# Kernel optimization log

Measured on AMD Instinct MI355X. Metric: run time of the kernel, lower is better.

The kernel has to match this reference:

```python
import jax, jax.numpy as jnp
import numpy as np


def setup_inputs() -> dict:
    key = jax.random.key(0)
    k0, k1, k2, k3, k4 = jax.random.split(key, 5)
    n, c, s, h, w = 4, 128, 31, 32, 22
    x = jax.random.normal(k0, (n, c, s, h, w), dtype=jnp.float32)
    # 1x1 conv to a single channel == per-pixel dot over channels + scalar bias
    scale = 1.0 / np.sqrt(c).astype(np.float32)
    w1 = jax.random.normal(k1, (c,), dtype=jnp.float32) * scale
    b1 = jax.random.normal(k2, (), dtype=jnp.float32) * 0.01
    w2 = jax.random.normal(k3, (c,), dtype=jnp.float32) * scale
    b2 = jax.random.normal(k4, (), dtype=jnp.float32) * 0.01
    return {"x": x, "w1": w1, "b1": b1, "w2": w2, "b2": b2, "top_k": 16}


def reference(x, w1, b1, w2, b2, top_k):
    n, c, s, h, w = x.shape
    hw = h * w
    ns = n * (s - 1)
    # adjacent-frame pairs; 1x1 conv (C->1) as channel contraction
    X0 = jnp.einsum('ncshw,c->nshw', x[:, :, : s - 1], w1) + b1  # (n, s-1, h, w)
    X1 = jnp.einsum('ncshw,c->nshw', x[:, :, 1:], w2) + b2       # (n, s-1, h, w)
    X0 = X0.reshape(ns, hw)
    X1 = X1.reshape(ns, hw)
    # outer-product scores per frame pair, softmax over last dim
    attention = jax.nn.softmax(X0[:, :, None] * X1[:, None, :], axis=2)  # (ns, hw, hw)
    # top-k values along last dim -> (ns, hw, k); torch .view(ns, k, h, w)
    # is a raw row-major reinterpretation, so a plain reshape is faithful.
    vals, _ = jax.lax.top_k(attention, top_k)
    vals = vals.reshape(n, s - 1, top_k, h, w)
    # trans_out: (n, s-1, k, h, w) -> (n, k, s-1, h, w)
    return jnp.transpose(vals, (0, 2, 1, 3, 4))
```

## Files before the change

kernel.cpp:

```cpp
#include <hip/hip_runtime.h>
#include <math.h>

#define NB   4
#define C    128
#define S    31
#define HW   704
#define T    30
#define NS   120
#define K    16

__global__ __launch_bounds__(256) void conv_select_kernel(
    const float* __restrict__ x,
    const float* __restrict__ w1, const float* __restrict__ b1p,
    const float* __restrict__ w2, const float* __restrict__ b2p,
    float* __restrict__ A, float* __restrict__ B,
    float* __restrict__ ptop, float* __restrict__ pbot) {
  const int tid   = threadIdx.x;
  const int lane  = tid & 63;
  const int cg    = tid >> 6;
  const int fr    = blockIdx.x / 3;
  const int chunk = blockIdx.x % 3;
  const int sf    = fr % S;
  const int n     = fr / S;
  const int f4    = chunk * 64 + lane;
  const bool act  = f4 < 176;
  const int f4c   = act ? f4 : 175;

  const float4* xp =
      (const float4*)(x + (((size_t)(n * C + cg * 32) * S + sf) * HW)) + f4c;
  float4 a1 = make_float4(0.f, 0.f, 0.f, 0.f);
  float4 a2 = make_float4(0.f, 0.f, 0.f, 0.f);
#pragma unroll
  for (int c = 0; c < 32; ++c) {
    float4 xv = xp[(size_t)c * (S * HW / 4)];
    const float wa = w1[cg * 32 + c];
    const float wb = w2[cg * 32 + c];
    a1.x = fmaf(xv.x, wa, a1.x); a1.y = fmaf(xv.y, wa, a1.y);
    a1.z = fmaf(xv.z, wa, a1.z); a1.w = fmaf(xv.w, wa, a1.w);
    a2.x = fmaf(xv.x, wb, a2.x); a2.y = fmaf(xv.y, wb, a2.y);
    a2.z = fmaf(xv.z, wb, a2.z); a2.w = fmaf(xv.w, wb, a2.w);
  }
  __shared__ float4 s1[4][64];
  __shared__ float4 s2[4][64];
  s1[cg][lane] = a1;
  s2[cg][lane] = a2;
  __syncthreads();
  if (tid < 64) {
    float4 r1 = s1[0][tid], r2 = s2[0][tid];
#pragma unroll
    for (int u = 1; u < 4; ++u) {
      float4 t1 = s1[u][tid], t2 = s2[u][tid];
      r1.x += t1.x; r1.y += t1.y; r1.z += t1.z; r1.w += t1.w;
      r2.x += t2.x; r2.y += t2.y; r2.z += t2.z; r2.w += t2.w;
    }
    const float bb1 = b1p[0], bb2 = b2p[0];
    r1.x += bb1; r1.y += bb1; r1.z += bb1; r1.w += bb1;
    r2.x += bb2; r2.y += bb2; r2.z += bb2; r2.w += bb2;
    const bool act2 = (chunk * 64 + tid) < 176;
    if (act2) {
      if (sf < T)
        ((float4*)(A + (size_t)(n * T + sf) * HW))[chunk * 64 + tid] = r1;
      if (sf >= 1)
        ((float4*)(B + (size_t)(n * T + sf - 1) * HW))[chunk * 64 + tid] = r2;
    }
    s2[0][tid] = r2;
  }
  __syncthreads();

  if (tid < 64 && sf >= 1) {
    const int i = n * T + sf - 1;
    const int nv = (chunk == 2) ? 3 : 4;
    const float* bs = (const float*)&s2[0][0];
    float vt[4], vb[4];
#pragma unroll
    for (int j = 0; j < 3; ++j) {
      const float v = bs[j * 64 + tid];
      vt[j] = v; vb[j] = v;
    }
    if (nv == 4) { const float v = bs[192 + tid]; vt[3] = v; vb[3] = v; }
    else         { vt[3] = -INFINITY;         vb[3] = INFINITY; }
    float* pt = ptop + (i * 3 + chunk) * K;
    float* pb = pbot + (i * 3 + chunk) * K;
#pragma unroll 1
    for (int rr = 0; rr < K; ++rr) {
      float lmT = fmaxf(fmaxf(vt[0], vt[1]), fmaxf(vt[2], vt[3]));
      float lmB = fminf(fminf(vb[0], vb[1]), fminf(vb[2], vb[3]));
      float gT = lmT, gB = lmB;
#pragma unroll
      for (int off = 1; off < 64; off <<= 1) {
        gT = fmaxf(gT, __shfl_xor(gT, off, 64));
        gB = fminf(gB, __shfl_xor(gB, off, 64));
      }
      const unsigned long long mT = __ballot(lmT == gT);
      const unsigned long long mB = __ballot(lmB == gB);
      if (tid == (int)(__ffsll(mT) - 1)) {
        bool done = false;
#pragma unroll
        for (int j = 0; j < 4; ++j) {
          const bool hit = (!done) && (vt[j] == gT);
          vt[j] = hit ? -INFINITY : vt[j];
          done  = done || hit;
        }
      }
      if (tid == (int)(__ffsll(mB) - 1)) {
        bool done = false;
#pragma unroll
        for (int j = 0; j < 4; ++j) {
          const bool hit = (!done) && (vb[j] == gB);
          vb[j] = hit ? INFINITY : vb[j];
          done  = done || hit;
        }
      }
      if (tid == 0) { pt[rr] = gT; pb[rr] = gB; }
    }
  }
}

__global__ __launch_bounds__(256) void softmax_merge_kernel(
    const float* __restrict__ A, const float* __restrict__ B,
    const float* __restrict__ ptop, const float* __restrict__ pbot,
    float* __restrict__ out) {
  __shared__ float4 bs4[176];
  __shared__ float  partial[4][64];
  __shared__ float  seltop[K], selbot[K];
  const int tid  = threadIdx.x;
  const int lane = tid & 63;
  const int w    = tid >> 6;
  const int i    = blockIdx.x / 11;
  const int slab = blockIdx.x % 11;
  const int n    = i / T;
  const int tp   = i % T;

  if (tid < 176) bs4[tid] = ((const float4*)(B + i * HW))[tid];
  const int   r = slab * 64 + lane;
  const float a = A[i * HW + r];

  if (w == 0) {
    const float* pt = ptop + i * 3 * K;
    float e = -INFINITY;
    if (lane < 16)       e = pt[lane];
    else if (lane < 32)  e = pt[47 - lane];
#pragma unroll
    for (int off = 16; off >= 1; off >>= 1) {
      const float xx = __shfl_xor(e, off, 64);
      e = (lane & off) ? fminf(e, xx) : fmaxf(e, xx);
    }
    if (lane >= 32)      e = -INFINITY;
    else if (lane >= 16) e = pt[63 - lane];
#pragma unroll
    for (int off = 16; off >= 1; off >>= 1) {
      const float xx = __shfl_xor(e, off, 64);
      e = (lane & off) ? fminf(e, xx) : fmaxf(e, xx);
    }
    if (lane < 16) seltop[lane] = e;
  } else if (w == 1) {
    const float* pb = pbot + i * 3 * K;
    float e = INFINITY;
    if (lane < 16)       e = pb[lane];
    else if (lane < 32)  e = pb[47 - lane];
#pragma unroll
    for (int off = 16; off >= 1; off >>= 1) {
      const float xx = __shfl_xor(e, off, 64);
      e = (lane & off) ? fmaxf(e, xx) : fminf(e, xx);
    }
    if (lane >= 32)      e = INFINITY;
    else if (lane >= 16) e = pb[63 - lane];
#pragma unroll
    for (int off = 16; off >= 1; off >>= 1) {
      const float xx = __shfl_xor(e, off, 64);
      e = (lane & off) ? fmaxf(e, xx) : fminf(e, xx);
    }
    if (lane < 16) selbot[lane] = e;
  }
  __syncthreads();

  const float st0 = seltop[0];
  const float sb0 = selbot[0];
  const float L2E = 1.4426950408889634f;
  const float a2  = a * L2E;
  const float nm  = -((a >= 0.f) ? a * st0 : a * sb0) * L2E;

  float p0 = 0.f, p1 = 0.f, p2 = 0.f, p3 = 0.f;
#pragma unroll 11
  for (int j = 0; j < 44; ++j) {
    const float4 bq = bs4[w * 44 + j];
    p0 += __builtin_amdgcn_exp2f(fmaf(a2, bq.x, nm));
    p1 += __builtin_amdgcn_exp2f(fmaf(a2, bq.y, nm));
    p2 += __builtin_amdgcn_exp2f(fmaf(a2, bq.z, nm));
    p3 += __builtin_amdgcn_exp2f(fmaf(a2, bq.w, nm));
  }
  partial[w][lane] = (p0 + p1) + (p2 + p3);
  __syncthreads();

  if (w == 0) {
    const float part =
        (partial[0][lane] + partial[1][lane]) +
        (partial[2][lane] + partial[3][lane]);
    const float rp = 1.f / part;
    float ov[16];
#pragma unroll
    for (int t = 0; t < K; ++t) {
      const float sel = (a >= 0.f) ? seltop[t] : selbot[t];
      ov[t] = __builtin_amdgcn_exp2f(fmaf(a2, sel, nm)) * rp;
    }
    float* op = out + (((size_t)(n * K + r / 44)) * T + tp) * HW + (r % 44) * K;
#pragma unroll
    for (int t4 = 0; t4 < 4; ++t4)
      ((float4*)op)[t4] = ((const float4*)ov)[t4];
  }
}

extern "C" void kernel_launch(void* const* d_in, const int* in_sizes, int n_in,
                              void* d_out, int out_size, void* d_ws, size_t ws_size,
                              hipStream_t stream) {
  (void)in_sizes; (void)n_in; (void)out_size; (void)ws_size;
  const float* x  = (const float*)d_in[0];
  const float* w1 = (const float*)d_in[1];
  const float* b1 = (const float*)d_in[2];
  const float* w2 = (const float*)d_in[3];
  const float* b2 = (const float*)d_in[4];
  float* out = (float*)d_out;

  float* A    = (float*)d_ws;
  float* B    = A + NS * HW;
  float* ptop = B + NS * HW;
  float* pbot = ptop + NS * 3 * K;

  conv_select_kernel<<<372, 256, 0, stream>>>(x, w1, b1, w2, b2,
                                              A, B, ptop, pbot);
  softmax_merge_kernel<<<NS * 11, 256, 0, stream>>>(A, B, ptop, pbot, out);
}
```

Before: 107.5 us.

## Fuse conv/select and softmax kernels into one cooperative launch with grid sync

Merges the two kernels into a single cooperative kernel that runs the conv/partial-top-k phase on the first 372 blocks, then uses a grid-wide barrier before every block runs the softmax/merge phase. Shared memory for the two phases is overlaid in a union. This aims to remove the second kernel launch and the gap between launches. The cost is a grid.sync over 1320 blocks, which requires all blocks to be co-resident, plus the latency of the barrier itself. If the cooperative launch fails, the code falls back to the original two launches.

```diff
diff --git a/kernel.cpp b/kernel.cpp
--- a/kernel.cpp
+++ b/kernel.cpp
@@ -1,5 +1,8 @@
 #include <hip/hip_runtime.h>
+#include <hip/hip_cooperative_groups.h>
 #include <math.h>
+
+namespace cg = cooperative_groups;
 
 #define NB   4
 #define C    128
@@ -8,6 +11,212 @@
 #define T    30
 #define NS   120
 #define K    16
+#define CONVB 372
+#define GRID  (NS * 11)
+
+__global__ __launch_bounds__(256) void fused_kernel(
+    const float* __restrict__ x,
+    const float* __restrict__ w1, const float* __restrict__ b1p,
+    const float* __restrict__ w2, const float* __restrict__ b2p,
+    float* __restrict__ A, float* __restrict__ B,
+    float* __restrict__ ptop, float* __restrict__ pbot,
+    float* __restrict__ out) {
+  __shared__ union {
+    struct { float4 s1[4][64]; float4 s2[4][64]; } p1;
+    struct {
+      float4 bs4[176];
+      float  partial[4][64];
+      float  seltop[K], selbot[K];
+    } p2;
+  } sm;
+  cg::grid_group grid = cg::this_grid();
+  const int tid  = threadIdx.x;
+  const int lane = tid & 63;
+
+  if (blockIdx.x < CONVB) {
+    const int cg_   = tid >> 6;
+    const int fr    = blockIdx.x / 3;
+    const int chunk = blockIdx.x % 3;
+    const int sf    = fr % S;
+    const int n     = fr / S;
+    const int f4    = chunk * 64 + lane;
+    const int f4c   = (f4 < 176) ? f4 : 175;
+
+    const float4* xp =
+        (const float4*)(x + (((size_t)(n * C + cg_ * 32) * S + sf) * HW)) + f4c;
+    float4 a1 = make_float4(0.f, 0.f, 0.f, 0.f);
+    float4 a2 = make_float4(0.f, 0.f, 0.f, 0.f);
+#pragma unroll
+    for (int c = 0; c < 32; ++c) {
+      float4 xv = xp[(size_t)c * (S * HW / 4)];
+      const float wa = w1[cg_ * 32 + c];
+      const float wb = w2[cg_ * 32 + c];
+      a1.x = fmaf(xv.x, wa, a1.x); a1.y = fmaf(xv.y, wa, a1.y);
+      a1.z = fmaf(xv.z, wa, a1.z); a1.w = fmaf(xv.w, wa, a1.w);
+      a2.x = fmaf(xv.x, wb, a2.x); a2.y = fmaf(xv.y, wb, a2.y);
+      a2.z = fmaf(xv.z, wb, a2.z); a2.w = fmaf(xv.w, wb, a2.w);
+    }
+    sm.p1.s1[cg_][lane] = a1;
+    sm.p1.s2[cg_][lane] = a2;
+    __syncthreads();
+    if (tid < 64) {
+      float4 r1 = sm.p1.s1[0][tid], r2 = sm.p1.s2[0][tid];
+#pragma unroll
+      for (int u = 1; u < 4; ++u) {
+        float4 t1 = sm.p1.s1[u][tid], t2 = sm.p1.s2[u][tid];
+        r1.x += t1.x; r1.y += t1.y; r1.z += t1.z; r1.w += t1.w;
+        r2.x += t2.x; r2.y += t2.y; r2.z += t2.z; r2.w += t2.w;
+      }
+      const float bb1 = b1p[0], bb2 = b2p[0];
+      r1.x += bb1; r1.y += bb1; r1.z += bb1; r1.w += bb1;
+      r2.x += bb2; r2.y += bb2; r2.z += bb2; r2.w += bb2;
+      if ((chunk * 64 + tid) < 176) {
+        if (sf < T)
+          ((float4*)(A + (size_t)(n * T + sf) * HW))[chunk * 64 + tid] = r1;
+        if (sf >= 1)
+          ((float4*)(B + (size_t)(n * T + sf - 1) * HW))[chunk * 64 + tid] = r2;
+      }
+      sm.p1.s2[0][tid] = r2;
+    }
+    __syncthreads();
+
+    if (tid < 64 && sf >= 1) {
+      const int i  = n * T + sf - 1;
+      const int nv = (chunk == 2) ? 3 : 4;
+      const float* bs = (const float*)&sm.p1.s2[0][0];
+      float vt[4], vb[4];
+#pragma unroll
+      for (int j = 0; j < 3; ++j) {
+        const float v = bs[j * 64 + tid];
+        vt[j] = v; vb[j] = v;
+      }
+      if (nv == 4) { const float v = bs[192 + tid]; vt[3] = v; vb[3] = v; }
+      else         { vt[3] = -INFINITY;         vb[3] = INFINITY; }
+      float* pt = ptop + (i * 3 + chunk) * K;
+      float* pb = pbot + (i * 3 + chunk) * K;
+#pragma unroll 1
+      for (int rr = 0; rr < K; ++rr) {
+        float lmT = fmaxf(fmaxf(vt[0], vt[1]), fmaxf(vt[2], vt[3]));
+        float lmB = fminf(fminf(vb[0], vb[1]), fminf(vb[2], vb[3]));
+        float gT = lmT, gB = lmB;
+#pragma unroll
+        for (int off = 1; off < 64; off <<= 1) {
+          gT = fmaxf(gT, __shfl_xor(gT, off, 64));
+          gB = fminf(gB, __shfl_xor(gB, off, 64));
+        }
+        const unsigned long long mT = __ballot(lmT == gT);
+        const unsigned long long mB = __ballot(lmB == gB);
+        if (tid == (int)(__ffsll(mT) - 1)) {
+          bool done = false;
+#pragma unroll
+          for (int j = 0; j < 4; ++j) {
+            const bool hit = (!done) && (vt[j] == gT);
+            vt[j] = hit ? -INFINITY : vt[j];
+            done  = done || hit;
+          }
+        }
+        if (tid == (int)(__ffsll(mB) - 1)) {
+          bool done = false;
+#pragma unroll
+          for (int j = 0; j < 4; ++j) {
+            const bool hit = (!done) && (vb[j] == gB);
+            vb[j] = hit ? INFINITY : vb[j];
+            done  = done || hit;
+          }
+        }
+        if (tid == 0) { pt[rr] = gT; pb[rr] = gB; }
+      }
+    }
+  }
+
+  grid.sync();
+
+  {
+    const int w    = tid >> 6;
+    const int i    = blockIdx.x / 11;
+    const int slab = blockIdx.x % 11;
+    const int n    = i / T;
+    const int tp   = i % T;
+
+    if (tid < 176) sm.p2.bs4[tid] = ((const float4*)(B + i * HW))[tid];
+    const int   r = slab * 64 + lane;
+    const float a = A[i * HW + r];
+
+    if (w == 0) {
+      const float* pt = ptop + i * 3 * K;
+      float e = -INFINITY;
+      if (lane < 16)       e = pt[lane];
+      else if (lane < 32)  e = pt[47 - lane];
+#pragma unroll
+      for (int off = 16; off >= 1; off >>= 1) {
+        const float xx = __shfl_xor(e, off, 64);
+        e = (lane & off) ? fminf(e, xx) : fmaxf(e, xx);
+      }
+      if (lane >= 32)      e = -INFINITY;
+      else if (lane >= 16) e = pt[63 - lane];
+#pragma unroll
+      for (int off = 16; off >= 1; off >>= 1) {
+        const float xx = __shfl_xor(e, off, 64);
+        e = (lane & off) ? fminf(e, xx) : fmaxf(e, xx);
+      }
+      if (lane < 16) sm.p2.seltop[lane] = e;
+    } else if (w == 1) {
+      const float* pb = pbot + i * 3 * K;
+      float e = INFINITY;
+      if (lane < 16)       e = pb[lane];
+      else if (lane < 32)  e = pb[47 - lane];
+#pragma unroll
+      for (int off = 16; off >= 1; off >>= 1) {
+        const float xx = __shfl_xor(e, off, 64);
+        e = (lane & off) ? fmaxf(e, xx) : fminf(e, xx);
+      }
+      if (lane >= 32)      e = INFINITY;
+      else if (lane >= 16) e = pb[63 - lane];
+#pragma unroll
+      for (int off = 16; off >= 1; off >>= 1) {
+        const float xx = __shfl_xor(e, off, 64);
+        e = (lane & off) ? fmaxf(e, xx) : fminf(e, xx);
+      }
+      if (lane < 16) sm.p2.selbot[lane] = e;
+    }
+    __syncthreads();
+
+    const float st0 = sm.p2.seltop[0];
+    const float sb0 = sm.p2.selbot[0];
+    const float L2E = 1.4426950408889634f;
+    const float a2  = a * L2E;
+    const float nm  = -((a >= 0.f) ? a * st0 : a * sb0) * L2E;
+
+    float p0 = 0.f, p1 = 0.f, p2 = 0.f, p3 = 0.f;
+#pragma unroll 11
+    for (int j = 0; j < 44; ++j) {
+      const float4 bq = sm.p2.bs4[w * 44 + j];
+      p0 += __builtin_amdgcn_exp2f(fmaf(a2, bq.x, nm));
+      p1 += __builtin_amdgcn_exp2f(fmaf(a2, bq.y, nm));
+      p2 += __builtin_amdgcn_exp2f(fmaf(a2, bq.z, nm));
+      p3 += __builtin_amdgcn_exp2f(fmaf(a2, bq.w, nm));
+    }
+    sm.p2.partial[w][lane] = (p0 + p1) + (p2 + p3);
+    __syncthreads();
+
+    if (w == 0) {
+      const float part =
+          (sm.p2.partial[0][lane] + sm.p2.partial[1][lane]) +
+          (sm.p2.partial[2][lane] + sm.p2.partial[3][lane]);
+      const float rp = 1.f / part;
+      float ov[16];
+#pragma unroll
+      for (int t = 0; t < K; ++t) {
+        const float sel = (a >= 0.f) ? sm.p2.seltop[t] : sm.p2.selbot[t];
+        ov[t] = __builtin_amdgcn_exp2f(fmaf(a2, sel, nm)) * rp;
+      }
+      float* op = out + (((size_t)(n * K + r / 44)) * T + tp) * HW + (r % 44) * K;
+#pragma unroll
+      for (int t4 = 0; t4 < 4; ++t4)
+        ((float4*)op)[t4] = ((const float4*)ov)[t4];
+    }
+  }
+}
 
 __global__ __launch_bounds__(256) void conv_select_kernel(
     const float* __restrict__ x,
@@ -17,24 +226,23 @@
     float* __restrict__ ptop, float* __restrict__ pbot) {
   const int tid   = threadIdx.x;
   const int lane  = tid & 63;
-  const int cg    = tid >> 6;
+  const int cg_   = tid >> 6;
   const int fr    = blockIdx.x / 3;
   const int chunk = blockIdx.x % 3;
   const int sf    = fr % S;
   const int n     = fr / S;
   const int f4    = chunk * 64 + lane;
-  const bool act  = f4 < 176;
-  const int f4c   = act ? f4 : 175;
+  const int f4c   = (f4 < 176) ? f4 : 175;
 
   const float4* xp =
-      (const float4*)(x + (((size_t)(n * C + cg * 32) * S + sf) * HW)) + f4c;
+      (const float4*)(x + (((size_t)(n * C + cg_ * 32) * S + sf) * HW)) + f4c;
   float4 a1 = make_float4(0.f, 0.f, 0.f, 0.f);
   float4 a2 = make_float4(0.f, 0.f, 0.f, 0.f);
 #pragma unroll
   for (int c = 0; c < 32; ++c) {
     float4 xv = xp[(size_t)c * (S * HW / 4)];
-    const float wa = w1[cg * 32 + c];
-    const float wb = w2[cg * 32 + c];
+    const float wa = w1[cg_ * 32 + c];
+    const float wb = w2[cg_ * 32 + c];
     a1.x = fmaf(xv.x, wa, a1.x); a1.y = fmaf(xv.y, wa, a1.y);
     a1.z = fmaf(xv.z, wa, a1.z); a1.w = fmaf(xv.w, wa, a1.w);
     a2.x = fmaf(xv.x, wb, a2.x); a2.y = fmaf(xv.y, wb, a2.y);
@@ -42,8 +250,8 @@
   }
   __shared__ float4 s1[4][64];
   __shared__ float4 s2[4][64];
-  s1[cg][lane] = a1;
-  s2[cg][lane] = a2;
+  s1[cg_][lane] = a1;
+  s2[cg_][lane] = a2;
   __syncthreads();
   if (tid < 64) {
     float4 r1 = s1[0][tid], r2 = s2[0][tid];
@@ -56,8 +264,7 @@
     const float bb1 = b1p[0], bb2 = b2p[0];
     r1.x += bb1; r1.y += bb1; r1.z += bb1; r1.w += bb1;
     r2.x += bb2; r2.y += bb2; r2.z += bb2; r2.w += bb2;
-    const bool act2 = (chunk * 64 + tid) < 176;
-    if (act2) {
+    if ((chunk * 64 + tid) < 176) {
       if (sf < T)
         ((float4*)(A + (size_t)(n * T + sf) * HW))[chunk * 64 + tid] = r1;
       if (sf >= 1)
@@ -68,7 +275,7 @@
   __syncthreads();
 
   if (tid < 64 && sf >= 1) {
-    const int i = n * T + sf - 1;
+    const int i  = n * T + sf - 1;
     const int nv = (chunk == 2) ? 3 : 4;
     const float* bs = (const float*)&s2[0][0];
     float vt[4], vb[4];
@@ -226,7 +433,14 @@
   float* ptop = B + NS * HW;
   float* pbot = ptop + NS * 3 * K;
 
-  conv_select_kernel<<<372, 256, 0, stream>>>(x, w1, b1, w2, b2,
-                                              A, B, ptop, pbot);
-  softmax_merge_kernel<<<NS * 11, 256, 0, stream>>>(A, B, ptop, pbot, out);
+  void* args[] = {(void*)&x, (void*)&w1, (void*)&b1, (void*)&w2, (void*)&b2,
+                  (void*)&A, (void*)&B, (void*)&ptop, (void*)&pbot,
+                  (void*)&out};
+  hipError_t err = hipLaunchCooperativeKernel(
+      (void*)fused_kernel, dim3(GRID), dim3(256), args, 0, stream);
+  if (err != hipSuccess) {
+    conv_select_kernel<<<CONVB, 256, 0, stream>>>(x, w1, b1, w2, b2,
+                                                  A, B, ptop, pbot);
+    softmax_merge_kernel<<<GRID, 256, 0, stream>>>(A, B, ptop, pbot, out);
+  }
 }
```

Result: slower. 269.3 us (+150.6%).
